# Optimization experiments

Measured on AMD Instinct MI355X. Metric: run time of the kernel, lower is better.

Reference implementation:

```python
import jax, jax.numpy as jnp
import numpy as np

SELF_TOPK_RATE = 0.05
LN_EPS = 1e-5


def _forward(q, k, v, fc_w, fc_b, ln_g, ln_b):
    # q, k, v: [B, S, D] (original code transposes to seq-first; math is identical batch-first)
    b, s, d = q.shape
    scale = d ** -0.5
    logits = jnp.einsum('bqd,bkd->bqk', q, k) * scale              # [B,S,S]
    # glbal_mask: self-similarity of keys, column-summed, top-k selection
    raw_self = jnp.einsum('bqd,bkd->bqk', k, k) * scale            # [B,S,S]
    w = raw_self.sum(axis=1)                                        # sum over dim=-2 -> [B,S]
    topk = max(1, int(s * SELF_TOPK_RATE))                          # static
    _, topk_idx = jax.lax.top_k(w, topk)                            # [B,topk]
    sel = jnp.zeros((b, s), dtype=bool).at[jnp.arange(b)[:, None], topk_idx].set(True)
    cmax = logits.max(axis=(1, 2))                                  # [B]
    w_mapped = jnp.where(sel, cmax[:, None], -cmax[:, None] / 3.0)  # [B,S]
    final = jax.nn.softmax(logits + w_mapped[:, None, :], axis=-1)  # [B,S,S]
    # Original einsum 'bqs,bkd->bqd' contracts s and k INDEPENDENTLY:
    # attn[b,q,d] = (sum_s final[b,q,s]) * (sum_k v[b,k,d])
    attn = final.sum(-1)[:, :, None] * v.sum(1)[:, None, :]         # [B,S,D]
    attn = jnp.nan_to_num(attn, nan=0.0, posinf=1e5, neginf=-1e5)
    h = attn @ fc_w.T + fc_b                                        # Linear; dropout = identity (eval)
    x = h + q                                                       # residual
    mu = x.mean(-1, keepdims=True)
    var = ((x - mu) ** 2).mean(-1, keepdims=True)
    return (x - mu) * jax.lax.rsqrt(var + LN_EPS) * ln_g + ln_b     # [B,S,D]


def setup_inputs() -> dict:
    key = jax.random.key(0)
    ks = jax.random.split(key, 5)
    B, S, D = 8, 2048, 768
    q = jax.random.normal(ks[0], (B, S, D), jnp.float32)
    k = jax.random.normal(ks[1], (B, S, D), jnp.float32)
    v = jax.random.normal(ks[2], (B, S, D), jnp.float32)
    mask = jnp.zeros((B, S), dtype=bool)  # unused in the original math path
    index = jnp.arange(B, dtype=jnp.int32)  # unused
    fc_w = jax.random.normal(ks[3], (D, D), jnp.float32) * 0.02
    fc_b = jnp.zeros((D,), jnp.float32)
    ln_g = jnp.ones((D,), jnp.float32)
    ln_b = jnp.zeros((D,), jnp.float32)
    return {"q": q, "k": k, "v": v, "mask": mask, "fc_w": fc_w, "fc_b": fc_b,
            "ln_g": ln_g, "ln_b": ln_b, "index": index, "typeAdd_Del": 1}


def reference(q, k, v, mask, fc_w, fc_b, ln_g, ln_b, index, typeAdd_Del):
    # mask, index, typeAdd_Del are accepted but unused by the original forward math
    return _forward(q, k, v, fc_w, fc_b, ln_g, ln_b)
```

## Files before the change

### kernel.cpp

```cpp
#include <hip/hip_runtime.h>

#define NB 8
#define NS 2048
#define ND 768
#define ND4 192
#define SC 128
#define ROWS_PER_CHUNK (NS / SC)

typedef float f4 __attribute__((ext_vector_type(4)));

__global__ __launch_bounds__(192) void vpart_kernel(const float* __restrict__ v,
                                                    float* __restrict__ part) {
    const int c = blockIdx.x;
    const int b = blockIdx.y;
    const int t = threadIdx.x;
    const f4* v4 = (const f4*)v + ((size_t)b * NS + (size_t)c * ROWS_PER_CHUNK) * ND4 + t;
    f4 acc = (f4)(0.f);
#pragma unroll
    for (int i = 0; i < ROWS_PER_CHUNK; ++i) {
        f4 x = __builtin_nontemporal_load(v4 + (size_t)i * ND4);
        acc += x;
    }
    ((f4*)part)[((size_t)c * NB + b) * ND4 + t] = acc;
}

__global__ __launch_bounds__(256) void vreduce_kernel(const float* __restrict__ part,
                                                      float* __restrict__ vsum) {
    const int i = blockIdx.x * 256 + threadIdx.x;
    float acc = 0.f;
#pragma unroll 8
    for (int c = 0; c < SC; ++c) acc += part[(size_t)c * (NB * ND) + i];
    vsum[i] = acc;
}

__global__ __launch_bounds__(256) void matvec_kernel(const float* __restrict__ fcw,
                                                     const float* __restrict__ fcb,
                                                     const float* __restrict__ vsum,
                                                     float* __restrict__ hvec) {
    __shared__ float lds[NB * ND];
    const int t = threadIdx.x;
    for (int i = t; i < NB * ND4; i += 256)
        ((f4*)lds)[i] = ((const f4*)vsum)[i];
    __syncthreads();

    const int w = t >> 6, l = t & 63;
    const int d = blockIdx.x * 4 + w;
    const f4* wrow = (const f4*)(fcw + (size_t)d * ND);
    float acc[NB] = {};
#pragma unroll
    for (int k = 0; k < 3; ++k) {
        const int e4 = l + k * 64;
        const f4 wv = wrow[e4];
#pragma unroll
        for (int b = 0; b < NB; ++b) {
            const f4 vs = ((const f4*)lds)[b * ND4 + e4];
            acc[b] += wv.x * vs.x + wv.y * vs.y + wv.z * vs.z + wv.w * vs.w;
        }
    }
#pragma unroll
    for (int off = 32; off >= 1; off >>= 1)
#pragma unroll
        for (int b = 0; b < NB; ++b)
            acc[b] += __shfl_down(acc[b], off, 64);
    if (l == 0) {
        const float bias = fcb[d];
#pragma unroll
        for (int b = 0; b < NB; ++b) hvec[b * ND + d] = acc[b] + bias;
    }
}

__global__ __launch_bounds__(256) void ln_kernel(const float* __restrict__ q,
                                                 const float* __restrict__ hvec,
                                                 const float* __restrict__ lng,
                                                 const float* __restrict__ lnb,
                                                 float* __restrict__ out) {
    const int w = threadIdx.x >> 6, l = threadIdx.x & 63;
    const int r0 = blockIdx.x * 8 + (w << 1);
    const int b = r0 >> 11;
    const f4* qa = (const f4*)q + (size_t)r0 * ND4;
    const f4* qb = qa + ND4;
    const f4* h4 = (const f4*)hvec + (size_t)b * ND4;

    f4 xa[3], xb[3];
    float sa = 0.f, sqa = 0.f, sb = 0.f, sqb = 0.f;
#pragma unroll
    for (int k = 0; k < 3; ++k) {
        const int e4 = l + k * 64;
        const f4 qva = __builtin_nontemporal_load(qa + e4);
        const f4 qvb = __builtin_nontemporal_load(qb + e4);
        const f4 hv  = h4[e4];
        const f4 va = qva + hv;
        const f4 vb = qvb + hv;
        xa[k] = va; xb[k] = vb;
        sa  += va.x + va.y + va.z + va.w;
        sqa += va.x * va.x + va.y * va.y + va.z * va.z + va.w * va.w;
        sb  += vb.x + vb.y + vb.z + vb.w;
        sqb += vb.x * vb.x + vb.y * vb.y + vb.z * vb.z + vb.w * vb.w;
    }
#pragma unroll
    for (int off = 32; off >= 1; off >>= 1) {
        sa  += __shfl_xor(sa,  off, 64);
        sqa += __shfl_xor(sqa, off, 64);
        sb  += __shfl_xor(sb,  off, 64);
        sqb += __shfl_xor(sqb, off, 64);
    }
    const float inv = 1.0f / (float)ND;
    const float ma = sa * inv, mb = sb * inv;
    const float ra = rsqrtf(sqa * inv - ma * ma + 1e-5f);
    const float rb = rsqrtf(sqb * inv - mb * mb + 1e-5f);

    f4* oa = (f4*)out + (size_t)r0 * ND4;
    f4* ob = oa + ND4;
#pragma unroll
    for (int k = 0; k < 3; ++k) {
        const int e4 = l + k * 64;
        const f4 gv = ((const f4*)lng)[e4];
        const f4 bv = ((const f4*)lnb)[e4];
        f4 ova, ovb;
        ova.x = (xa[k].x - ma) * ra * gv.x + bv.x;
        ova.y = (xa[k].y - ma) * ra * gv.y + bv.y;
        ova.z = (xa[k].z - ma) * ra * gv.z + bv.z;
        ova.w = (xa[k].w - ma) * ra * gv.w + bv.w;
        ovb.x = (xb[k].x - mb) * rb * gv.x + bv.x;
        ovb.y = (xb[k].y - mb) * rb * gv.y + bv.y;
        ovb.z = (xb[k].z - mb) * rb * gv.z + bv.z;
        ovb.w = (xb[k].w - mb) * rb * gv.w + bv.w;
        __builtin_nontemporal_store(ova, oa + e4);
        __builtin_nontemporal_store(ovb, ob + e4);
    }
}

extern "C" void kernel_launch(void* const* d_in, const int* in_sizes, int n_in,
                              void* d_out, int out_size, void* d_ws, size_t ws_size,
                              hipStream_t stream) {
    const float* q   = (const float*)d_in[0];
    const float* v   = (const float*)d_in[2];
    const float* fcw = (const float*)d_in[4];
    const float* fcb = (const float*)d_in[5];
    const float* lng = (const float*)d_in[6];
    const float* lnb = (const float*)d_in[7];
    float* out = (float*)d_out;

    float* part = (float*)d_ws;
    float* vsum = part + (size_t)SC * NB * ND;
    float* hvec = vsum + NB * ND;

    vpart_kernel<<<dim3(SC, NB), 192, 0, stream>>>(v, part);
    vreduce_kernel<<<(NB * ND) / 256, 256, 0, stream>>>(part, vsum);
    matvec_kernel<<<ND / 4, 256, 0, stream>>>(fcw, fcb, vsum, hvec);
    ln_kernel<<<(NB * NS) / 8, 256, 0, stream>>>(q, hvec, lng, lnb, out);
}
```

Before: 42.92 us.

## Fuse four stages into one cooperative kernel with grid syncs

Replaces the four separate launches (v partial sums, reduce, matvec, layernorm) with a single cooperative persistent kernel of 1024 blocks that uses grid.sync between stages. The aim is to remove per-launch overhead and inter-kernel gaps. The fallback path also drops the nontemporal loads and stores. Grid syncs add their own cost, and the occupancy query runs on every call.

Result: faster. 40.82 us (-4.9%).

```diff
diff --git a/kernel.cpp b/kernel.cpp
--- a/kernel.cpp
+++ b/kernel.cpp
@@ -1,26 +1,154 @@
 #include <hip/hip_runtime.h>
+#include <hip/hip_cooperative_groups.h>
+
+namespace cg = cooperative_groups;
 
 #define NB 8
 #define NS 2048
 #define ND 768
 #define ND4 192
 #define SC 128
-#define ROWS_PER_CHUNK (NS / SC)
+#define RPC 16
+#define GRID 1024
+#define TPB 256
 
 typedef float f4 __attribute__((ext_vector_type(4)));
+
+__global__ __launch_bounds__(TPB, 4) void fused_kernel(
+    const float* __restrict__ q, const float* __restrict__ v,
+    const float* __restrict__ fcw, const float* __restrict__ fcb,
+    const float* __restrict__ lng, const float* __restrict__ lnb,
+    float* __restrict__ part, float* __restrict__ vsum,
+    float* __restrict__ hvec, float* __restrict__ out) {
+    cg::grid_group grid = cg::this_grid();
+    const int bb = blockIdx.x;
+    const int t = threadIdx.x;
+
+    {
+        const int c = bb >> 3, b = bb & 7;
+        if (t < ND4) {
+            const f4* v4 = (const f4*)v + ((size_t)(b * NS + c * RPC)) * ND4 + t;
+            f4 acc = (f4)(0.f);
+#pragma unroll
+            for (int i = 0; i < RPC; ++i)
+                acc += __builtin_nontemporal_load(v4 + (size_t)i * ND4);
+            ((f4*)part)[(size_t)bb * ND4 + t] = acc;
+        }
+    }
+    grid.sync();
+
+    if (bb < 6) {
+        const int idx = bb * TPB + t;
+        const f4* p4 = (const f4*)part;
+        f4 acc = (f4)(0.f);
+#pragma unroll 8
+        for (int c = 0; c < SC; ++c) acc += p4[(size_t)c * 1536 + idx];
+        ((f4*)vsum)[idx] = acc;
+    }
+    grid.sync();
+
+    {
+        __shared__ float lds[NB * ND];
+        if (bb < 192) {
+            for (int i = t; i < NB * ND4; i += TPB)
+                ((f4*)lds)[i] = ((const f4*)vsum)[i];
+            __syncthreads();
+            const int w = t >> 6, l = t & 63;
+            const int d = bb * 4 + w;
+            const f4* wrow = (const f4*)(fcw + (size_t)d * ND);
+            float acc[NB] = {};
+#pragma unroll
+            for (int k = 0; k < 3; ++k) {
+                const int e4 = l + k * 64;
+                const f4 wv = wrow[e4];
+#pragma unroll
+                for (int b = 0; b < NB; ++b) {
+                    const f4 vs = ((const f4*)lds)[b * ND4 + e4];
+                    acc[b] += wv.x * vs.x + wv.y * vs.y + wv.z * vs.z + wv.w * vs.w;
+                }
+            }
+#pragma unroll
+            for (int off = 32; off >= 1; off >>= 1)
+#pragma unroll
+                for (int b = 0; b < NB; ++b)
+                    acc[b] += __shfl_down(acc[b], off, 64);
+            if (l == 0) {
+                const float bias = fcb[d];
+#pragma unroll
+                for (int b = 0; b < NB; ++b) hvec[b * ND + d] = acc[b] + bias;
+            }
+        }
+    }
+    grid.sync();
+
+    {
+        const int w = t >> 6, l = t & 63;
+#pragma unroll
+        for (int j = 0; j < 2; ++j) {
+            const int r0 = bb * 16 + w * 4 + j * 2;
+            const int b = r0 >> 11;
+            const f4* qa = (const f4*)q + (size_t)r0 * ND4;
+            const f4* qb = qa + ND4;
+            const f4* h4 = (const f4*)hvec + (size_t)b * ND4;
+
+            f4 xa[3], xb[3];
+            float sa = 0.f, sqa = 0.f, sb = 0.f, sqb = 0.f;
+#pragma unroll
+            for (int k = 0; k < 3; ++k) {
+                const int e4 = l + k * 64;
+                const f4 qva = __builtin_nontemporal_load(qa + e4);
+                const f4 qvb = __builtin_nontemporal_load(qb + e4);
+                const f4 hv  = h4[e4];
+                const f4 va = qva + hv;
+                const f4 vb = qvb + hv;
+                xa[k] = va; xb[k] = vb;
+                sa  += va.x + va.y + va.z + va.w;
+                sqa += va.x * va.x + va.y * va.y + va.z * va.z + va.w * va.w;
+                sb  += vb.x + vb.y + vb.z + vb.w;
+                sqb += vb.x * vb.x + vb.y * vb.y + vb.z * vb.z + vb.w * vb.w;
+            }
+#pragma unroll
+            for (int off = 32; off >= 1; off >>= 1) {
+                sa  += __shfl_xor(sa,  off, 64);
+                sqa += __shfl_xor(sqa, off, 64);
+                sb  += __shfl_xor(sb,  off, 64);
+                sqb += __shfl_xor(sqb, off, 64);
+            }
+            const float inv = 1.0f / (float)ND;
+            const float ma = sa * inv, mb = sb * inv;
+            const float ra = rsqrtf(sqa * inv - ma * ma + 1e-5f);
+            const float rb = rsqrtf(sqb * inv - mb * mb + 1e-5f);
+
+            f4* oa = (f4*)out + (size_t)r0 * ND4;
+            f4* ob = oa + ND4;
+#pragma unroll
+            for (int k = 0; k < 3; ++k) {
+                const int e4 = l + k * 64;
+                const f4 gv = ((const f4*)lng)[e4];
+                const f4 bv = ((const f4*)lnb)[e4];
+                f4 ova, ovb;
+                ova.x = (xa[k].x - ma) * ra * gv.x + bv.x;
+                ova.y = (xa[k].y - ma) * ra * gv.y + bv.y;
+                ova.z = (xa[k].z - ma) * ra * gv.z + bv.z;
+                ova.w = (xa[k].w - ma) * ra * gv.w + bv.w;
+                ovb.x = (xb[k].x - mb) * rb * gv.x + bv.x;
+                ovb.y = (xb[k].y - mb) * rb * gv.y + bv.y;
+                ovb.z = (xb[k].z - mb) * rb * gv.z + bv.z;
+                ovb.w = (xb[k].w - mb) * rb * gv.w + bv.w;
+                __builtin_nontemporal_store(ova, oa + e4);
+                __builtin_nontemporal_store(ovb, ob + e4);
+            }
+        }
+    }
+}
 
 __global__ __launch_bounds__(192) void vpart_kernel(const float* __restrict__ v,
                                                     float* __restrict__ part) {
-    const int c = blockIdx.x;
-    const int b = blockIdx.y;
-    const int t = threadIdx.x;
-    const f4* v4 = (const f4*)v + ((size_t)b * NS + (size_t)c * ROWS_PER_CHUNK) * ND4 + t;
+    const int c = blockIdx.x, b = blockIdx.y, t = threadIdx.x;
+    const f4* v4 = (const f4*)v + ((size_t)b * NS + (size_t)c * RPC) * ND4 + t;
     f4 acc = (f4)(0.f);
 #pragma unroll
-    for (int i = 0; i < ROWS_PER_CHUNK; ++i) {
-        f4 x = __builtin_nontemporal_load(v4 + (size_t)i * ND4);
-        acc += x;
-    }
+    for (int i = 0; i < RPC; ++i) acc += v4[(size_t)i * ND4];
     ((f4*)part)[((size_t)c * NB + b) * ND4 + t] = acc;
 }
 
@@ -42,7 +170,6 @@
     for (int i = t; i < NB * ND4; i += 256)
         ((f4*)lds)[i] = ((const f4*)vsum)[i];
     __syncthreads();
-
     const int w = t >> 6, l = t & 63;
     const int d = blockIdx.x * 4 + w;
     const f4* wrow = (const f4*)(fcw + (size_t)d * ND);
@@ -60,8 +187,7 @@
 #pragma unroll
     for (int off = 32; off >= 1; off >>= 1)
 #pragma unroll
-        for (int b = 0; b < NB; ++b)
-            acc[b] += __shfl_down(acc[b], off, 64);
+        for (int b = 0; b < NB; ++b) acc[b] += __shfl_down(acc[b], off, 64);
     if (l == 0) {
         const float bias = fcb[d];
 #pragma unroll
@@ -80,17 +206,13 @@
     const f4* qa = (const f4*)q + (size_t)r0 * ND4;
     const f4* qb = qa + ND4;
     const f4* h4 = (const f4*)hvec + (size_t)b * ND4;
-
     f4 xa[3], xb[3];
     float sa = 0.f, sqa = 0.f, sb = 0.f, sqb = 0.f;
 #pragma unroll
     for (int k = 0; k < 3; ++k) {
         const int e4 = l + k * 64;
-        const f4 qva = __builtin_nontemporal_load(qa + e4);
-        const f4 qvb = __builtin_nontemporal_load(qb + e4);
-        const f4 hv  = h4[e4];
-        const f4 va = qva + hv;
-        const f4 vb = qvb + hv;
+        const f4 qva = qa[e4], qvb = qb[e4], hv = h4[e4];
+        const f4 va = qva + hv, vb = qvb + hv;
         xa[k] = va; xb[k] = vb;
         sa  += va.x + va.y + va.z + va.w;
         sqa += va.x * va.x + va.y * va.y + va.z * va.z + va.w * va.w;
@@ -99,16 +221,13 @@
     }
 #pragma unroll
     for (int off = 32; off >= 1; off >>= 1) {
-        sa  += __shfl_xor(sa,  off, 64);
-        sqa += __shfl_xor(sqa, off, 64);
-        sb  += __shfl_xor(sb,  off, 64);
-        sqb += __shfl_xor(sqb, off, 64);
+        sa += __shfl_xor(sa, off, 64); sqa += __shfl_xor(sqa, off, 64);
+        sb += __shfl_xor(sb, off, 64); sqb += __shfl_xor(sqb, off, 64);
     }
     const float inv = 1.0f / (float)ND;
     const float ma = sa * inv, mb = sb * inv;
     const float ra = rsqrtf(sqa * inv - ma * ma + 1e-5f);
     const float rb = rsqrtf(sqb * inv - mb * mb + 1e-5f);
-
     f4* oa = (f4*)out + (size_t)r0 * ND4;
     f4* ob = oa + ND4;
 #pragma unroll
@@ -125,8 +244,7 @@
         ovb.y = (xb[k].y - mb) * rb * gv.y + bv.y;
         ovb.z = (xb[k].z - mb) * rb * gv.z + bv.z;
         ovb.w = (xb[k].w - mb) * rb * gv.w + bv.w;
-        __builtin_nontemporal_store(ova, oa + e4);
-        __builtin_nontemporal_store(ovb, ob + e4);
+        oa[e4] = ova; ob[e4] = ovb;
     }
 }
 
@@ -145,8 +263,26 @@
     float* vsum = part + (size_t)SC * NB * ND;
     float* hvec = vsum + NB * ND;
 
-    vpart_kernel<<<dim3(SC, NB), 192, 0, stream>>>(v, part);
-    vreduce_kernel<<<(NB * ND) / 256, 256, 0, stream>>>(part, vsum);
-    matvec_kernel<<<ND / 4, 256, 0, stream>>>(fcw, fcb, vsum, hvec);
-    ln_kernel<<<(NB * NS) / 8, 256, 0, stream>>>(q, hvec, lng, lnb, out);
-}
+    int blocksPerCU = 0;
+    (void)hipOccupancyMaxActiveBlocksPerMultiprocessor(&blocksPerCU,
+        (const void*)fused_kernel, TPB, 0);
+    static int numCU = 0;
+    if (numCU == 0) {
+        hipDeviceProp_t prop;
+        (void)hipGetDeviceProperties(&prop, 0);
+        numCU = prop.multiProcessorCount;
+    }
+
+    if (blocksPerCU * numCU >= GRID) {
+        void* args[] = {(void*)&q, (void*)&v, (void*)&fcw, (void*)&fcb,
+                        (void*)&lng, (void*)&lnb, (void*)&part, (void*)&vsum,
+                        (void*)&hvec, (void*)&out};
+        (void)hipLaunchCooperativeKernel((const void*)fused_kernel, dim3(GRID),
+                                         dim3(TPB), args, 0, stream);
+    } else {
+        vpart_kernel<<<dim3(SC, NB), 192, 0, stream>>>(v, part);
+        vreduce_kernel<<<(NB * ND) / 256, 256, 0, stream>>>(part, vsum);
+        matvec_kernel<<<ND / 4, 256, 0, stream>>>(fcw, fcb, vsum, hvec);
+        ln_kernel<<<(NB * NS) / 8, 256, 0, stream>>>(q, hvec, lng, lnb, out);
+    }
+}
```

## Fuse pipeline into single cooperative kernel with grid-wide syncs

Applied to the files above, without the earlier changes.

Replaces the four separate launches with one cooperative kernel of 1024 blocks. It uses grid.sync between the v partial-sum phase, a merged reduce-plus-matvec phase run on 64 blocks, and the layernorm phase. The aim is to remove launch gaps and one intermediate kernel. In exchange it adds grid-barrier costs and an occupancy query on every call, and it drops the nontemporal loads. A three-kernel fallback runs when the device cannot hold all 1024 blocks at once.

New measurement: 53.71 us. +25.1%, slower.

```diff
diff --git a/kernel.cpp b/kernel.cpp
--- a/kernel.cpp
+++ b/kernel.cpp
@@ -1,81 +1,71 @@
 #include <hip/hip_runtime.h>
+#include <hip/hip_cooperative_groups.h>
+
+namespace cg = cooperative_groups;
 
 #define NB 8
 #define NS 2048
 #define ND 768
 #define ND4 192
 #define SC 128
-#define ROWS_PER_CHUNK (NS / SC)
+#define RPC 16
+#define GRID 1024
+#define TPB 256
 
 typedef float f4 __attribute__((ext_vector_type(4)));
 
-__global__ __launch_bounds__(192) void vpart_kernel(const float* __restrict__ v,
-                                                    float* __restrict__ part) {
-    const int c = blockIdx.x;
-    const int b = blockIdx.y;
-    const int t = threadIdx.x;
-    const f4* v4 = (const f4*)v + ((size_t)b * NS + (size_t)c * ROWS_PER_CHUNK) * ND4 + t;
-    f4 acc = (f4)(0.f);
-#pragma unroll
-    for (int i = 0; i < ROWS_PER_CHUNK; ++i) {
-        f4 x = __builtin_nontemporal_load(v4 + (size_t)i * ND4);
-        acc += x;
-    }
-    ((f4*)part)[((size_t)c * NB + b) * ND4 + t] = acc;
-}
-
-__global__ __launch_bounds__(256) void vreduce_kernel(const float* __restrict__ part,
-                                                      float* __restrict__ vsum) {
-    const int i = blockIdx.x * 256 + threadIdx.x;
-    float acc = 0.f;
+
+__device__ __forceinline__ void phase_vpart(const float* __restrict__ v,
+                                            float* __restrict__ part,
+                                            int c, int b, int t) {
+    if (t < ND4) {
+        const f4* v4 = (const f4*)v + ((size_t)(b * NS + c * RPC)) * ND4 + t;
+        f4 acc = (f4)(0.f);
+#pragma unroll
+        for (int i = 0; i < RPC; ++i) acc += v4[(size_t)i * ND4];
+        ((f4*)part)[((size_t)c * NB + b) * ND4 + t] = acc;
+    }
+}
+
+__device__ __forceinline__ void phase_bc(const float* __restrict__ part,
+                                         const float* __restrict__ fcw,
+                                         const float* __restrict__ fcb,
+                                         float* __restrict__ hvec,
+                                         float* __restrict__ lds_vs,
+                                         int slab, int b, int t) {
+    if (t < ND4) {
+        const f4* p4 = (const f4*)part + (size_t)b * ND4 + t;
+        f4 acc = (f4)(0.f);
 #pragma unroll 8
-    for (int c = 0; c < SC; ++c) acc += part[(size_t)c * (NB * ND) + i];
-    vsum[i] = acc;
-}
-
-__global__ __launch_bounds__(256) void matvec_kernel(const float* __restrict__ fcw,
-                                                     const float* __restrict__ fcb,
-                                                     const float* __restrict__ vsum,
-                                                     float* __restrict__ hvec) {
-    __shared__ float lds[NB * ND];
-    const int t = threadIdx.x;
-    for (int i = t; i < NB * ND4; i += 256)
-        ((f4*)lds)[i] = ((const f4*)vsum)[i];
+        for (int c = 0; c < SC; ++c) acc += p4[(size_t)c * (NB * ND4)];
+        ((f4*)lds_vs)[t] = acc;
+    }
     __syncthreads();
-
     const int w = t >> 6, l = t & 63;
-    const int d = blockIdx.x * 4 + w;
-    const f4* wrow = (const f4*)(fcw + (size_t)d * ND);
-    float acc[NB] = {};
-#pragma unroll
-    for (int k = 0; k < 3; ++k) {
-        const int e4 = l + k * 64;
-        const f4 wv = wrow[e4];
-#pragma unroll
-        for (int b = 0; b < NB; ++b) {
-            const f4 vs = ((const f4*)lds)[b * ND4 + e4];
-            acc[b] += wv.x * vs.x + wv.y * vs.y + wv.z * vs.z + wv.w * vs.w;
+#pragma unroll 4
+    for (int i = 0; i < 24; ++i) {
+        const int d = slab * 96 + w * 24 + i;
+        const f4* wrow = (const f4*)(fcw + (size_t)d * ND);
+        float s = 0.f;
+#pragma unroll
+        for (int k = 0; k < 3; ++k) {
+            const int e4 = l + k * 64;
+            const f4 wv = wrow[e4];
+            const f4 vs = ((const f4*)lds_vs)[e4];
+            s += wv.x * vs.x + wv.y * vs.y + wv.z * vs.z + wv.w * vs.w;
         }
-    }
-#pragma unroll
-    for (int off = 32; off >= 1; off >>= 1)
-#pragma unroll
-        for (int b = 0; b < NB; ++b)
-            acc[b] += __shfl_down(acc[b], off, 64);
-    if (l == 0) {
-        const float bias = fcb[d];
-#pragma unroll
-        for (int b = 0; b < NB; ++b) hvec[b * ND + d] = acc[b] + bias;
-    }
-}
-
-__global__ __launch_bounds__(256) void ln_kernel(const float* __restrict__ q,
-                                                 const float* __restrict__ hvec,
-                                                 const float* __restrict__ lng,
-                                                 const float* __restrict__ lnb,
-                                                 float* __restrict__ out) {
-    const int w = threadIdx.x >> 6, l = threadIdx.x & 63;
-    const int r0 = blockIdx.x * 8 + (w << 1);
+#pragma unroll
+        for (int off = 32; off >= 1; off >>= 1) s += __shfl_xor(s, off, 64);
+        if (l == 0) hvec[b * ND + d] = s + fcb[d];
+    }
+}
+
+__device__ __forceinline__ void phase_ln2(const float* __restrict__ q,
+                                          const float* __restrict__ hvec,
+                                          const float* __restrict__ lng,
+                                          const float* __restrict__ lnb,
+                                          float* __restrict__ out,
+                                          int r0, int l) {
     const int b = r0 >> 11;
     const f4* qa = (const f4*)q + (size_t)r0 * ND4;
     const f4* qb = qa + ND4;
@@ -86,8 +76,8 @@
 #pragma unroll
     for (int k = 0; k < 3; ++k) {
         const int e4 = l + k * 64;
-        const f4 qva = __builtin_nontemporal_load(qa + e4);
-        const f4 qvb = __builtin_nontemporal_load(qb + e4);
+        const f4 qva = qa[e4];
+        const f4 qvb = qb[e4];
         const f4 hv  = h4[e4];
         const f4 va = qva + hv;
         const f4 vb = qvb + hv;
@@ -130,6 +120,53 @@
     }
 }
 
+__global__ __launch_bounds__(TPB, 4) void fused2_kernel(
+    const float* __restrict__ q, const float* __restrict__ v,
+    const float* __restrict__ fcw, const float* __restrict__ fcb,
+    const float* __restrict__ lng, const float* __restrict__ lnb,
+    float* __restrict__ part, float* __restrict__ hvec,
+    float* __restrict__ out) {
+    cg::grid_group grid = cg::this_grid();
+    __shared__ float lds_vs[ND];
+    const int bb = blockIdx.x;
+    const int t = threadIdx.x;
+
+    phase_vpart(v, part, bb >> 3, bb & 7, t);
+    grid.sync();
+
+    if (bb < 64) phase_bc(part, fcw, fcb, hvec, lds_vs, bb >> 3, bb & 7, t);
+    grid.sync();
+
+    {
+        const int w = t >> 6, l = t & 63;
+#pragma unroll
+        for (int j = 0; j < 2; ++j)
+            phase_ln2(q, hvec, lng, lnb, out, bb * 16 + w * 4 + j * 2, l);
+    }
+}
+
+__global__ __launch_bounds__(192) void vpart_kernel(const float* __restrict__ v,
+                                                    float* __restrict__ part) {
+    phase_vpart(v, part, blockIdx.x, blockIdx.y, threadIdx.x);
+}
+
+__global__ __launch_bounds__(TPB) void bc_kernel(const float* __restrict__ part,
+                                                 const float* __restrict__ fcw,
+                                                 const float* __restrict__ fcb,
+                                                 float* __restrict__ hvec) {
+    __shared__ float lds_vs[ND];
+    phase_bc(part, fcw, fcb, hvec, lds_vs, blockIdx.x >> 3, blockIdx.x & 7, threadIdx.x);
+}
+
+__global__ __launch_bounds__(TPB) void ln_kernel(const float* __restrict__ q,
+                                                 const float* __restrict__ hvec,
+                                                 const float* __restrict__ lng,
+                                                 const float* __restrict__ lnb,
+                                                 float* __restrict__ out) {
+    const int w = threadIdx.x >> 6, l = threadIdx.x & 63;
+    phase_ln2(q, hvec, lng, lnb, out, blockIdx.x * 8 + w * 2, l);
+}
+
 extern "C" void kernel_launch(void* const* d_in, const int* in_sizes, int n_in,
                               void* d_out, int out_size, void* d_ws, size_t ws_size,
                               hipStream_t stream) {
@@ -142,11 +179,27 @@
     float* out = (float*)d_out;
 
     float* part = (float*)d_ws;
-    float* vsum = part + (size_t)SC * NB * ND;
-    float* hvec = vsum + NB * ND;
-
-    vpart_kernel<<<dim3(SC, NB), 192, 0, stream>>>(v, part);
-    vreduce_kernel<<<(NB * ND) / 256, 256, 0, stream>>>(part, vsum);
-    matvec_kernel<<<ND / 4, 256, 0, stream>>>(fcw, fcb, vsum, hvec);
-    ln_kernel<<<(NB * NS) / 8, 256, 0, stream>>>(q, hvec, lng, lnb, out);
-}
+    float* hvec = part + (size_t)SC * NB * ND;
+
+    int blocksPerCU = 0;
+    (void)hipOccupancyMaxActiveBlocksPerMultiprocessor(&blocksPerCU,
+        (const void*)fused2_kernel, TPB, 0);
+    static int numCU = 0;
+    if (numCU == 0) {
+        hipDeviceProp_t prop;
+        (void)hipGetDeviceProperties(&prop, 0);
+        numCU = prop.multiProcessorCount;
+    }
+
+    if (blocksPerCU * numCU >= GRID) {
+        void* args[] = {(void*)&q, (void*)&v, (void*)&fcw, (void*)&fcb,
+                        (void*)&lng, (void*)&lnb, (void*)&part, (void*)&hvec,
+                        (void*)&out};
+        (void)hipLaunchCooperativeKernel((const void*)fused2_kernel, dim3(GRID),
+                                         dim3(TPB), args, 0, stream);
+    } else {
+        vpart_kernel<<<dim3(SC, NB), 192, 0, stream>>>(v, part);
+        bc_kernel<<<64, TPB, 0, stream>>>(part, fcw, fcb, hvec);
+        ln_kernel<<<(NB * NS) / 8, TPB, 0, stream>>>(q, hvec, lng, lnb, out);
+    }
+}
```
